# Kernel tuning notes

Hardware: AMD Instinct MI355X
Metric: run time of the kernel (lower is better)

The kernel has to match this reference:

```python
import jax, jax.numpy as jnp
import numpy as np

NUM_CLASSES = 80
TOPK = 9
EPS_OVERLAPS = 1e-6  # mmdet BboxOverlaps2D: union clamped to eps
EPS_YOLOV6 = 1e-9    # yolov6_iou_calculator: eps added to union


def _pairwise_iou(b1, b2, eps, add_eps):
    # b1: (..., M, 4), b2: (..., N, 4) xyxy -> (..., M, N)
    lt = jnp.maximum(b1[..., :, None, :2], b2[..., None, :, :2])
    rb = jnp.minimum(b1[..., :, None, 2:], b2[..., None, :, 2:])
    wh = jnp.clip(rb - lt, 0.0)
    overlap = wh[..., 0] * wh[..., 1]
    a1 = (b1[..., 2] - b1[..., 0]) * (b1[..., 3] - b1[..., 1])
    a2 = (b2[..., 2] - b2[..., 0]) * (b2[..., 3] - b2[..., 1])
    union = a1[..., :, None] + a2[..., None, :] - overlap
    return overlap / (union + eps) if add_eps else overlap / jnp.maximum(union, eps)


def _assign(pred_bboxes, priors, gt_labels, gt_bboxes, pad_bbox_flag, num_level_priors):
    num_level_priors = tuple(int(n) for n in np.asarray(num_level_priors))
    # priors (x, y, stride_w, stride_h) -> 5*stride cell boxes in xyxy
    cell_half = priors[:, 2:] * 2.5
    prior_boxes = jnp.concatenate([priors[:, :2] - cell_half, priors[:, :2] + cell_half], axis=-1)
    bs, num_gt = gt_bboxes.shape[0], gt_bboxes.shape[1]
    num_priors = priors.shape[0]
    gt_flat = gt_bboxes.reshape(-1, 4)

    # step 1: IoU between all priors and all gts
    overlaps = _pairwise_iou(gt_flat, prior_boxes, EPS_OVERLAPS, False).reshape(bs, num_gt, num_priors)

    # step 2: center distances
    gt_cxy = (gt_flat[:, :2] + gt_flat[:, 2:]) * 0.5
    prior_cxy = (prior_boxes[:, :2] + prior_boxes[:, 2:]) * 0.5
    dist = jnp.sqrt(jnp.sum((gt_cxy[:, None, :] - prior_cxy[None, :, :]) ** 2, axis=-1))
    dist = dist.reshape(bs, num_gt, num_priors)

    # step 3: per-level topk closest candidates
    pad_bool = pad_bbox_flag[..., 0] > 0  # (bs, num_gt)
    b_ix = jnp.arange(bs)[:, None, None]
    g_ix = jnp.arange(num_gt)[None, :, None]
    is_in_list, cand_list = [], []
    start = 0
    for pl in num_level_priors:
        k = min(TOPK, pl)
        d_l = jax.lax.dynamic_slice_in_dim(dist, start, pl, axis=-1)
        _, idx = jax.lax.top_k(-d_l, k)  # (bs, num_gt, k) smallest distances
        cand_list.append(idx + start)
        idx_m = jnp.where(pad_bool[..., None], idx, 0)
        counts = jnp.zeros((bs, num_gt, pl), dist.dtype).at[b_ix, g_ix, idx_m].add(1.0)
        is_in_list.append(jnp.where(counts > 1, jnp.zeros_like(counts), counts))
        start += pl
    is_in_candidate = jnp.concatenate(is_in_list, axis=-1)   # (bs, num_gt, num_priors)
    candidate_idxs = jnp.concatenate(cand_list, axis=-1)     # (bs, num_gt, k*levels)

    # step 4: mean + std of candidate IoUs as threshold
    candidate_overlaps = jnp.where(is_in_candidate > 0, overlaps, jnp.zeros_like(overlaps))
    gathered = jnp.take_along_axis(candidate_overlaps, candidate_idxs, axis=-1)
    thr = jnp.mean(gathered, axis=-1, keepdims=True) + jnp.std(gathered, axis=-1, keepdims=True, ddof=1)

    # step 5: keep candidates above threshold
    is_pos = jnp.where(candidate_overlaps > thr, is_in_candidate, jnp.zeros_like(is_in_candidate))

    # step 6: center of prior must lie inside gt box
    lt = prior_cxy[None, None, :, :] - gt_bboxes[:, :, None, :2]
    rb = gt_bboxes[:, :, None, 2:] - prior_cxy[None, None, :, :]
    is_in_gts = (jnp.minimum(lt, rb).min(axis=-1) > 1e-9).astype(gt_bboxes.dtype)

    pos_mask = is_pos * is_in_gts * pad_bbox_flag  # pad flag broadcasts (bs,num_gt,1)

    # resolve priors assigned to multiple gts: keep highest IoU gt
    fg = pos_mask.sum(axis=-2)  # (bs, num_priors)
    best_gt = jnp.argmax(overlaps, axis=1)  # (bs, num_priors)
    is_max = jax.nn.one_hot(best_gt, num_gt, dtype=pos_mask.dtype).transpose(0, 2, 1)
    pos_mask = jnp.where(fg[:, None, :] > 1, is_max, pos_mask)
    fg_mask = pos_mask.sum(axis=-2)                 # (bs, num_priors)
    gt_idx = jnp.argmax(pos_mask, axis=-2)          # (bs, num_priors)

    # targets
    flat_idx = gt_idx + jnp.arange(bs)[:, None] * num_gt
    assigned_labels = gt_labels.reshape(-1)[flat_idx]
    assigned_labels = jnp.where(fg_mask > 0, assigned_labels, NUM_CLASSES)
    assigned_bboxes = gt_bboxes.reshape(-1, 4)[flat_idx]
    assigned_scores = jax.nn.one_hot(assigned_labels, NUM_CLASSES + 1, dtype=gt_bboxes.dtype)[..., :NUM_CLASSES]

    # weight scores by IoU with predictions
    ious = _pairwise_iou(gt_bboxes, pred_bboxes, EPS_YOLOV6, True) * pos_mask
    assigned_scores = assigned_scores * jnp.max(ious, axis=-2)[..., None]
    return assigned_labels, assigned_bboxes, assigned_scores, fg_mask > 0


def setup_inputs() -> dict:
    key = jax.random.key(0)
    k0, k1, k2, k3, k4 = jax.random.split(key, 5)
    bs, num_gt, img = 32, 64, 640
    strides = (8, 16, 32)
    pri = []
    for s in strides:
        n = img // s
        xs = (np.arange(n, dtype=np.float32) + 0.5) * s
        gy, gx = np.meshgrid(xs, xs, indexing='ij')
        pts = np.stack([gx.ravel(), gy.ravel()], axis=1)
        st = np.full((pts.shape[0], 2), s, dtype=np.float32)
        pri.append(np.concatenate([pts, st], axis=1))
    priors = jnp.asarray(np.concatenate(pri, axis=0))  # (8400, 4)
    num_level_priors = (6400, 1600, 400)
    num_priors = priors.shape[0]
    cxy = jax.random.uniform(k0, (bs, num_gt, 2), minval=50.0, maxval=590.0)
    wh = jax.random.uniform(k1, (bs, num_gt, 2), minval=20.0, maxval=200.0)
    gt_bboxes = jnp.concatenate([cxy - wh * 0.5, cxy + wh * 0.5], axis=-1)
    gt_labels = jax.random.randint(k2, (bs, num_gt, 1), 0, NUM_CLASSES)
    pad_bbox_flag = jnp.ones((bs, num_gt, 1), jnp.float32)
    pcxy = priors[None, :, :2] + jax.random.normal(k3, (bs, num_priors, 2)) * 4.0
    pwh = jax.random.uniform(k4, (bs, num_priors, 2), minval=10.0, maxval=150.0)
    pred_bboxes = jnp.concatenate([pcxy - pwh * 0.5, pcxy + pwh * 0.5], axis=-1)
    return {'pred_bboxes': pred_bboxes, 'priors': priors, 'gt_labels': gt_labels,
            'gt_bboxes': gt_bboxes, 'pad_bbox_flag': pad_bbox_flag,
            'num_level_priors': num_level_priors}


def reference(pred_bboxes, priors, gt_labels, gt_bboxes, pad_bbox_flag, num_level_priors):
    return _assign(pred_bboxes, priors, gt_labels, gt_bboxes, pad_bbox_flag, num_level_priors)
```

## Files before the change

kernel.cpp:

```cpp
#include <hip/hip_runtime.h>

#define BS 32
#define NG 64
#define NP 8400
#define NTOPK 9
#define NUM_CLASSES 80
#define NCAND 27

__device__ __forceinline__ unsigned long long wave_min_u64(unsigned long long k) {
    #pragma unroll
    for (int off = 1; off < 64; off <<= 1) {
        unsigned long long o = __shfl_xor(k, off, 64);
        k = (o < k) ? o : k;
    }
    return k;
}

__global__ __launch_bounds__(256) void k_candidates(
    const float4* __restrict__ gt_bboxes,
    const float*  __restrict__ pad_flag,
    unsigned long long* __restrict__ posbits
) {
    const int bg   = (blockIdx.x * 256 + threadIdx.x) >> 6;
    const int lane = threadIdx.x & 63;
    const int b  = bg >> 6;
    const int g  = bg & 63;

    const float4 gt  = gt_bboxes[bg];
    const float  pad = pad_flag[bg];
    const float  gcx = (gt.x + gt.z) * 0.5f;
    const float  gcy = (gt.y + gt.w) * 0.5f;
    const float  garea = (gt.z - gt.x) * (gt.w - gt.y);

    const float lvl_s[3] = {8.0f, 16.0f, 32.0f};
    const int   lvl_n[3] = {80, 40, 20};
    const int   lvl_b[3] = {0, 6400, 8000};

    float ov[NCAND];
    int   ixs[NCAND];

    float sum = 0.0f;

    const int dy5 = lane / 5;
    const int dx5 = lane - dy5 * 5;

    #pragma unroll
    for (int L = 0; L < 3; ++L) {
        const float s    = lvl_s[L];
        const int   n    = lvl_n[L];
        const int   base = lvl_b[L];

        int wx = (int)floorf(gcx / s) - 2;
        int wy = (int)floorf(gcy / s) - 2;
        wx = min(max(wx, 0), n - 5);
        wy = min(max(wy, 0), n - 5);

        unsigned long long key = ~0ull;
        if (lane < 25) {
            const int   iy  = wy + dy5;
            const int   ix  = wx + dx5;
            const float py  = ((float)iy + 0.5f) * s;
            const float px  = ((float)ix + 0.5f) * s;
            const float ddx = gcx - px;
            const float ddy = gcy - py;
            const float d   = sqrtf(ddx * ddx + ddy * ddy);
            key = ((unsigned long long)__float_as_uint(d) << 32) |
                  (unsigned int)(base + iy * n + ix);
        }

        const float hx = s * 2.5f;
        #pragma unroll
        for (int q = 0; q < NTOPK; ++q) {
            const unsigned long long m = wave_min_u64(key);
            if (key == m) key = ~0ull;

            const int slot = L * NTOPK + q;
            const int idx  = (int)(m & 0xffffffffu);
            const int rel  = idx - base;
            const int iy   = rel / n;
            const int ix   = rel - iy * n;
            const float px = ((float)ix + 0.5f) * s;
            const float py = ((float)iy + 0.5f) * s;
            const float px0 = px - hx, py0 = py - hx;
            const float px1 = px + hx, py1 = py + hx;
            float lx = fmaxf(gt.x, px0), ly = fmaxf(gt.y, py0);
            float rx = fminf(gt.z, px1), ry = fminf(gt.w, py1);
            float w = fmaxf(rx - lx, 0.0f), h = fmaxf(ry - ly, 0.0f);
            float ovl = w * h;
            float parea = (px1 - px0) * (py1 - py0);
            float o = ovl / fmaxf(garea + parea - ovl, 1e-6f);
            ov[slot]  = o;
            ixs[slot] = idx;
            sum += o;
        }
    }

    const float mean = sum / (float)NCAND;
    float var = 0.0f;
    #pragma unroll
    for (int i = 0; i < NCAND; ++i) {
        float d = ov[i] - mean;
        var += d * d;
    }
    const float thr = mean + sqrtf(var / (float)(NCAND - 1));

    if (pad > 0.0f && lane == 0) {
        #pragma unroll
        for (int i = 0; i < NCAND; ++i) {
            if (ov[i] > thr) {
                const int   L    = i / NTOPK;
                const float s    = lvl_s[L];
                const int   n    = lvl_n[L];
                const int   base = lvl_b[L];
                const int idx = ixs[i];
                const int rel = idx - base;
                const int iy  = rel / n;
                const int ix  = rel - iy * n;
                const float px = ((float)ix + 0.5f) * s;
                const float py = ((float)iy + 0.5f) * s;
                float mm = fminf(fminf(px - gt.x, py - gt.y),
                                 fminf(gt.z - px, gt.w - py));
                if (mm > 1e-9f) {
                    atomicOr(&posbits[(size_t)b * NP + idx], 1ull << g);
                }
            }
        }
    }
}

__global__ __launch_bounds__(256) void k_assign(
    const float4* __restrict__ priors,
    const float4* __restrict__ gt_bboxes,
    const int*    __restrict__ gt_labels,
    const float4* __restrict__ pred_bboxes,
    const unsigned long long* __restrict__ posbits,
    float* __restrict__ out)
{
    __shared__ float4 s_gt[NG];
    __shared__ int    s_lab[NG];
    __shared__ int    s_plab[256];
    __shared__ float  s_piou[256];

    const int b   = blockIdx.y;
    const int tid = threadIdx.x;
    if (tid < NG) {
        s_gt[tid]  = gt_bboxes[b * NG + tid];
        s_lab[tid] = gt_labels[b * NG + tid];
    }
    __syncthreads();

    const int p0 = blockIdx.x * 256;
    const int p  = p0 + tid;
    int   label  = NUM_CLASSES;
    float iou_w  = 0.0f;

    if (p < NP) {
        const size_t bp = (size_t)b * NP + p;
        unsigned long long mask = posbits[bp];
        int fg = __popcll(mask);
        int gidx = 0;

        if (fg > 1) {
            float4 pr = priors[p];
            float hx = pr.z * 2.5f, hy = pr.w * 2.5f;
            float px0 = pr.x - hx, py0 = pr.y - hy, px1 = pr.x + hx, py1 = pr.y + hy;
            float parea = (px1 - px0) * (py1 - py0);
            float best = -1.0f;
            for (int gg = 0; gg < NG; ++gg) {
                float4 gtb = s_gt[gg];
                float lx = fmaxf(gtb.x, px0), ly = fmaxf(gtb.y, py0);
                float rx = fminf(gtb.z, px1), ry = fminf(gtb.w, py1);
                float w = fmaxf(rx - lx, 0.0f), h = fmaxf(ry - ly, 0.0f);
                float ovl = w * h;
                float ga = (gtb.z - gtb.x) * (gtb.w - gtb.y);
                float v = ovl / fmaxf(ga + parea - ovl, 1e-6f);
                if (v > best) { best = v; gidx = gg; }
            }
        } else if (fg == 1) {
            gidx = __ffsll((unsigned long long)mask) - 1;
        }

        const bool  fgm = fg > 0;
        const float4 gtb = s_gt[gidx];
        label = fgm ? s_lab[gidx] : NUM_CLASSES;

        if (fgm) {
            float4 pb = pred_bboxes[bp];
            float lx = fmaxf(gtb.x, pb.x), ly = fmaxf(gtb.y, pb.y);
            float rx = fminf(gtb.z, pb.z), ry = fminf(gtb.w, pb.w);
            float w = fmaxf(rx - lx, 0.0f), h = fmaxf(ry - ly, 0.0f);
            float ov = w * h;
            float ga = (gtb.z - gtb.x) * (gtb.w - gtb.y);
            float pa = (pb.z - pb.x) * (pb.w - pb.y);
            iou_w = ov / (ga + pa - ov + 1e-9f);
        }

        out[bp] = (float)label;
        ((float4*)(out + (size_t)BS * NP))[bp] = gtb;
        out[(size_t)BS * NP * 85 + bp] = fgm ? 1.0f : 0.0f;
    }

    s_plab[tid] = label;
    s_piou[tid] = iou_w;
    __syncthreads();

    const int npr  = min(256, NP - p0);
    const int nfl4 = npr * 20;
    float4* o4 = (float4*)(out + (size_t)BS * NP * 5 + ((size_t)b * NP + p0) * 80);
    for (int q = tid; q < nfl4; q += 256) {
        int pl   = q / 20;
        int comp = q - pl * 20;
        int lab  = s_plab[pl];
        float iw = s_piou[pl];
        int dd = lab - comp * 4;
        float4 v;
        v.x = (dd == 0) ? iw : 0.0f;
        v.y = (dd == 1) ? iw : 0.0f;
        v.z = (dd == 2) ? iw : 0.0f;
        v.w = (dd == 3) ? iw : 0.0f;
        o4[q] = v;
    }
}

extern "C" void kernel_launch(void* const* d_in, const int* in_sizes, int n_in,
                              void* d_out, int out_size, void* d_ws, size_t ws_size,
                              hipStream_t stream) {
    const float4* pred_bboxes = (const float4*)d_in[0];
    const float4* priors      = (const float4*)d_in[1];
    const int*    gt_labels   = (const int*)d_in[2];
    const float4* gt_bboxes   = (const float4*)d_in[3];
    const float*  pad_flag    = (const float*)d_in[4];

    unsigned long long* posbits = (unsigned long long*)d_ws;
    hipMemsetAsync(posbits, 0, (size_t)BS * NP * sizeof(unsigned long long), stream);

    k_candidates<<<dim3(BS * NG * 64 / 256), dim3(256), 0, stream>>>(
        gt_bboxes, pad_flag, posbits);

    k_assign<<<dim3((NP + 255) / 256, BS), dim3(256), 0, stream>>>(
        priors, gt_bboxes, gt_labels, pred_bboxes, posbits, (float*)d_out);
}
```

Before: 129.4 us.

## Fuse memset, candidate selection and assignment into one cooperative kernel

Replaces the memset plus two kernel launches with a single cooperative kernel. It zeroes the bitmask in-kernel, runs candidate selection, and after a grid-wide sync performs assignment on 525-prior chunks per block. The wave-min reduction is also narrowed to 32 lanes, since only 25 lanes hold keys. This removes launch and memset overhead at the cost of two grid syncs and a fixed 512-block grid, which must all be co-resident.

```diff
diff --git a/kernel.cpp b/kernel.cpp
--- a/kernel.cpp
+++ b/kernel.cpp
@@ -1,4 +1,7 @@
 #include <hip/hip_runtime.h>
+#include <hip/hip_cooperative_groups.h>
+
+namespace cg = cooperative_groups;
 
 #define BS 32
 #define NG 64
@@ -7,154 +10,161 @@
 #define NUM_CLASSES 80
 #define NCAND 27
 
-__device__ __forceinline__ unsigned long long wave_min_u64(unsigned long long k) {
+#define NBLK 512
+#define NTHR 256
+#define CHUNK 525
+
+__device__ __forceinline__ unsigned long long wave_min_u64_32(unsigned long long k) {
     #pragma unroll
-    for (int off = 1; off < 64; off <<= 1) {
+    for (int off = 1; off < 32; off <<= 1) {
         unsigned long long o = __shfl_xor(k, off, 64);
         k = (o < k) ? o : k;
     }
     return k;
 }
 
-__global__ __launch_bounds__(256) void k_candidates(
+__global__ __launch_bounds__(NTHR, 2) void k_fused(
     const float4* __restrict__ gt_bboxes,
     const float*  __restrict__ pad_flag,
-    unsigned long long* __restrict__ posbits
-) {
-    const int bg   = (blockIdx.x * 256 + threadIdx.x) >> 6;
-    const int lane = threadIdx.x & 63;
-    const int b  = bg >> 6;
-    const int g  = bg & 63;
-
-    const float4 gt  = gt_bboxes[bg];
-    const float  pad = pad_flag[bg];
-    const float  gcx = (gt.x + gt.z) * 0.5f;
-    const float  gcy = (gt.y + gt.w) * 0.5f;
-    const float  garea = (gt.z - gt.x) * (gt.w - gt.y);
-
-    const float lvl_s[3] = {8.0f, 16.0f, 32.0f};
-    const int   lvl_n[3] = {80, 40, 20};
-    const int   lvl_b[3] = {0, 6400, 8000};
-
-    float ov[NCAND];
-    int   ixs[NCAND];
-
-    float sum = 0.0f;
-
-    const int dy5 = lane / 5;
-    const int dx5 = lane - dy5 * 5;
-
-    #pragma unroll
-    for (int L = 0; L < 3; ++L) {
-        const float s    = lvl_s[L];
-        const int   n    = lvl_n[L];
-        const int   base = lvl_b[L];
-
-        int wx = (int)floorf(gcx / s) - 2;
-        int wy = (int)floorf(gcy / s) - 2;
-        wx = min(max(wx, 0), n - 5);
-        wy = min(max(wy, 0), n - 5);
-
-        unsigned long long key = ~0ull;
-        if (lane < 25) {
-            const int   iy  = wy + dy5;
-            const int   ix  = wx + dx5;
-            const float py  = ((float)iy + 0.5f) * s;
-            const float px  = ((float)ix + 0.5f) * s;
-            const float ddx = gcx - px;
-            const float ddy = gcy - py;
-            const float d   = sqrtf(ddx * ddx + ddy * ddy);
-            key = ((unsigned long long)__float_as_uint(d) << 32) |
-                  (unsigned int)(base + iy * n + ix);
-        }
-
-        const float hx = s * 2.5f;
+    const float4* __restrict__ priors,
+    const int*    __restrict__ gt_labels,
+    const float4* __restrict__ pred_bboxes,
+    unsigned long long* __restrict__ posbits,
+    float* __restrict__ out)
+{
+    cg::grid_group grid = cg::this_grid();
+
+    __shared__ float4 s_gt[NG];
+    __shared__ int    s_lab[NG];
+    __shared__ int    s_plab[CHUNK];
+    __shared__ float  s_piou[CHUNK];
+
+    const int tid  = threadIdx.x;
+    const int gtid = blockIdx.x * NTHR + tid;
+
+    for (int i = gtid; i < BS * NP; i += NBLK * NTHR) posbits[i] = 0;
+    grid.sync();
+
+    {
+        const int bg   = gtid >> 6;
+        const int lane = tid & 63;
+        const int b  = bg >> 6;
+        const int g  = bg & 63;
+
+        const float4 gt  = gt_bboxes[bg];
+        const float  pad = pad_flag[bg];
+        const float  gcx = (gt.x + gt.z) * 0.5f;
+        const float  gcy = (gt.y + gt.w) * 0.5f;
+        const float  garea = (gt.z - gt.x) * (gt.w - gt.y);
+
+        const float lvl_s[3] = {8.0f, 16.0f, 32.0f};
+        const int   lvl_n[3] = {80, 40, 20};
+        const int   lvl_b[3] = {0, 6400, 8000};
+
+        float ov[NCAND];
+        int   ixs[NCAND];
+        float sum = 0.0f;
+
+        const int dy5 = lane / 5;
+        const int dx5 = lane - dy5 * 5;
+
         #pragma unroll
-        for (int q = 0; q < NTOPK; ++q) {
-            const unsigned long long m = wave_min_u64(key);
-            if (key == m) key = ~0ull;
-
-            const int slot = L * NTOPK + q;
-            const int idx  = (int)(m & 0xffffffffu);
-            const int rel  = idx - base;
-            const int iy   = rel / n;
-            const int ix   = rel - iy * n;
-            const float px = ((float)ix + 0.5f) * s;
-            const float py = ((float)iy + 0.5f) * s;
-            const float px0 = px - hx, py0 = py - hx;
-            const float px1 = px + hx, py1 = py + hx;
-            float lx = fmaxf(gt.x, px0), ly = fmaxf(gt.y, py0);
-            float rx = fminf(gt.z, px1), ry = fminf(gt.w, py1);
-            float w = fmaxf(rx - lx, 0.0f), h = fmaxf(ry - ly, 0.0f);
-            float ovl = w * h;
-            float parea = (px1 - px0) * (py1 - py0);
-            float o = ovl / fmaxf(garea + parea - ovl, 1e-6f);
-            ov[slot]  = o;
-            ixs[slot] = idx;
-            sum += o;
-        }
-    }
-
-    const float mean = sum / (float)NCAND;
-    float var = 0.0f;
-    #pragma unroll
-    for (int i = 0; i < NCAND; ++i) {
-        float d = ov[i] - mean;
-        var += d * d;
-    }
-    const float thr = mean + sqrtf(var / (float)(NCAND - 1));
-
-    if (pad > 0.0f && lane == 0) {
+        for (int L = 0; L < 3; ++L) {
+            const float s    = lvl_s[L];
+            const int   n    = lvl_n[L];
+            const int   base = lvl_b[L];
+
+            int wx = (int)floorf(gcx / s) - 2;
+            int wy = (int)floorf(gcy / s) - 2;
+            wx = min(max(wx, 0), n - 5);
+            wy = min(max(wy, 0), n - 5);
+
+            unsigned long long key = ~0ull;
+            if (lane < 25) {
+                const int   iy  = wy + dy5;
+                const int   ix  = wx + dx5;
+                const float py  = ((float)iy + 0.5f) * s;
+                const float px  = ((float)ix + 0.5f) * s;
+                const float ddx = gcx - px;
+                const float ddy = gcy - py;
+                const float d   = sqrtf(ddx * ddx + ddy * ddy);
+                key = ((unsigned long long)__float_as_uint(d) << 32) |
+                      (unsigned int)(base + iy * n + ix);
+            }
+
+            const float hx = s * 2.5f;
+            #pragma unroll
+            for (int q = 0; q < NTOPK; ++q) {
+                const unsigned long long m = wave_min_u64_32(key);
+                if (key == m) key = ~0ull;
+
+                const int slot = L * NTOPK + q;
+                const int idx  = (int)(m & 0xffffffffu);
+                const int rel  = idx - base;
+                const int iy   = rel / n;
+                const int ix   = rel - iy * n;
+                const float px = ((float)ix + 0.5f) * s;
+                const float py = ((float)iy + 0.5f) * s;
+                const float px0 = px - hx, py0 = py - hx;
+                const float px1 = px + hx, py1 = py + hx;
+                float lx = fmaxf(gt.x, px0), ly = fmaxf(gt.y, py0);
+                float rx = fminf(gt.z, px1), ry = fminf(gt.w, py1);
+                float w = fmaxf(rx - lx, 0.0f), h = fmaxf(ry - ly, 0.0f);
+                float ovl = w * h;
+                float parea = (px1 - px0) * (py1 - py0);
+                float o = ovl / fmaxf(garea + parea - ovl, 1e-6f);
+                ov[slot]  = o;
+                ixs[slot] = idx;
+                sum += o;
+            }
+        }
+
+        const float mean = sum / (float)NCAND;
+        float var = 0.0f;
         #pragma unroll
         for (int i = 0; i < NCAND; ++i) {
-            if (ov[i] > thr) {
-                const int   L    = i / NTOPK;
-                const float s    = lvl_s[L];
-                const int   n    = lvl_n[L];
-                const int   base = lvl_b[L];
-                const int idx = ixs[i];
-                const int rel = idx - base;
-                const int iy  = rel / n;
-                const int ix  = rel - iy * n;
-                const float px = ((float)ix + 0.5f) * s;
-                const float py = ((float)iy + 0.5f) * s;
-                float mm = fminf(fminf(px - gt.x, py - gt.y),
-                                 fminf(gt.z - px, gt.w - py));
-                if (mm > 1e-9f) {
-                    atomicOr(&posbits[(size_t)b * NP + idx], 1ull << g);
+            float d = ov[i] - mean;
+            var += d * d;
+        }
+        const float thr = mean + sqrtf(var / (float)(NCAND - 1));
+
+        if (pad > 0.0f && lane == 0) {
+            #pragma unroll
+            for (int i = 0; i < NCAND; ++i) {
+                if (ov[i] > thr) {
+                    const int   L    = i / NTOPK;
+                    const float s    = lvl_s[L];
+                    const int   n    = lvl_n[L];
+                    const int   base = lvl_b[L];
+                    const int idx = ixs[i];
+                    const int rel = idx - base;
+                    const int iy  = rel / n;
+                    const int ix  = rel - iy * n;
+                    const float px = ((float)ix + 0.5f) * s;
+                    const float py = ((float)iy + 0.5f) * s;
+                    float mm = fminf(fminf(px - gt.x, py - gt.y),
+                                     fminf(gt.z - px, gt.w - py));
+                    if (mm > 1e-9f) {
+                        atomicOr(&posbits[(size_t)b * NP + idx], 1ull << g);
+                    }
                 }
             }
         }
     }
-}
-
-__global__ __launch_bounds__(256) void k_assign(
-    const float4* __restrict__ priors,
-    const float4* __restrict__ gt_bboxes,
-    const int*    __restrict__ gt_labels,
-    const float4* __restrict__ pred_bboxes,
-    const unsigned long long* __restrict__ posbits,
-    float* __restrict__ out)
-{
-    __shared__ float4 s_gt[NG];
-    __shared__ int    s_lab[NG];
-    __shared__ int    s_plab[256];
-    __shared__ float  s_piou[256];
-
-    const int b   = blockIdx.y;
-    const int tid = threadIdx.x;
+    grid.sync();
+
+    const int b     = blockIdx.x >> 4;
+    const int chunk = blockIdx.x & 15;
+    const int pbase = chunk * CHUNK;
+
     if (tid < NG) {
         s_gt[tid]  = gt_bboxes[b * NG + tid];
         s_lab[tid] = gt_labels[b * NG + tid];
     }
     __syncthreads();
 
-    const int p0 = blockIdx.x * 256;
-    const int p  = p0 + tid;
-    int   label  = NUM_CLASSES;
-    float iou_w  = 0.0f;
-
-    if (p < NP) {
+    for (int pl = tid; pl < CHUNK; pl += NTHR) {
+        const int p = pbase + pl;
         const size_t bp = (size_t)b * NP + p;
         unsigned long long mask = posbits[bp];
         int fg = __popcll(mask);
@@ -180,9 +190,10 @@
             gidx = __ffsll((unsigned long long)mask) - 1;
         }
 
-        const bool  fgm = fg > 0;
+        const bool   fgm = fg > 0;
         const float4 gtb = s_gt[gidx];
-        label = fgm ? s_lab[gidx] : NUM_CLASSES;
+        const int  label = fgm ? s_lab[gidx] : NUM_CLASSES;
+        float iou_w = 0.0f;
 
         if (fgm) {
             float4 pb = pred_bboxes[bp];
@@ -198,16 +209,14 @@
         out[bp] = (float)label;
         ((float4*)(out + (size_t)BS * NP))[bp] = gtb;
         out[(size_t)BS * NP * 85 + bp] = fgm ? 1.0f : 0.0f;
-    }
-
-    s_plab[tid] = label;
-    s_piou[tid] = iou_w;
+
+        s_plab[pl] = label;
+        s_piou[pl] = iou_w;
+    }
     __syncthreads();
 
-    const int npr  = min(256, NP - p0);
-    const int nfl4 = npr * 20;
-    float4* o4 = (float4*)(out + (size_t)BS * NP * 5 + ((size_t)b * NP + p0) * 80);
-    for (int q = tid; q < nfl4; q += 256) {
+    float4* o4 = (float4*)(out + (size_t)BS * NP * 5 + ((size_t)b * NP + pbase) * 80);
+    for (int q = tid; q < CHUNK * 20; q += NTHR) {
         int pl   = q / 20;
         int comp = q - pl * 20;
         int lab  = s_plab[pl];
@@ -232,11 +241,12 @@
     const float*  pad_flag    = (const float*)d_in[4];
 
     unsigned long long* posbits = (unsigned long long*)d_ws;
-    hipMemsetAsync(posbits, 0, (size_t)BS * NP * sizeof(unsigned long long), stream);
-
-    k_candidates<<<dim3(BS * NG * 64 / 256), dim3(256), 0, stream>>>(
-        gt_bboxes, pad_flag, posbits);
-
-    k_assign<<<dim3((NP + 255) / 256, BS), dim3(256), 0, stream>>>(
-        priors, gt_bboxes, gt_labels, pred_bboxes, posbits, (float*)d_out);
+    float* out = (float*)d_out;
+
+    void* args[] = {
+        (void*)&gt_bboxes, (void*)&pad_flag, (void*)&priors,
+        (void*)&gt_labels, (void*)&pred_bboxes, (void*)&posbits, (void*)&out
+    };
+    hipLaunchCooperativeKernel((const void*)k_fused, dim3(NBLK), dim3(NTHR),
+                               args, 0, stream);
 }
```

Result: slower. 230.9 us (+78.5%).

## Replace global posbits bitmask with compact candidate list scattered in shared memory

Applied to the files above, without the earlier changes.

The candidate kernel now writes a compact list of positive prior indices per gt (27 entries) instead of doing global atomicOr into a per-prior 64-bit mask. This removes the memset of the mask buffer and the global atomics. The assign kernel rebuilds each tile's masks in shared memory by scanning the whole candidate list for its batch, which adds redundant reads per block. The wave reduction also shrinks to 32 lanes, since only 25 lanes hold keys.

```diff
diff --git a/kernel.cpp b/kernel.cpp
--- a/kernel.cpp
+++ b/kernel.cpp
@@ -7,9 +7,9 @@
 #define NUM_CLASSES 80
 #define NCAND 27
 
-__device__ __forceinline__ unsigned long long wave_min_u64(unsigned long long k) {
+__device__ __forceinline__ unsigned long long wave_min_u64_32(unsigned long long k) {
     #pragma unroll
-    for (int off = 1; off < 64; off <<= 1) {
+    for (int off = 1; off < 32; off <<= 1) {
         unsigned long long o = __shfl_xor(k, off, 64);
         k = (o < k) ? o : k;
     }
@@ -19,12 +19,10 @@
 __global__ __launch_bounds__(256) void k_candidates(
     const float4* __restrict__ gt_bboxes,
     const float*  __restrict__ pad_flag,
-    unsigned long long* __restrict__ posbits
-) {
+    unsigned int* __restrict__ cand)
+{
     const int bg   = (blockIdx.x * 256 + threadIdx.x) >> 6;
     const int lane = threadIdx.x & 63;
-    const int b  = bg >> 6;
-    const int g  = bg & 63;
 
     const float4 gt  = gt_bboxes[bg];
     const float  pad = pad_flag[bg];
@@ -38,7 +36,6 @@
 
     float ov[NCAND];
     int   ixs[NCAND];
-
     float sum = 0.0f;
 
     const int dy5 = lane / 5;
@@ -71,7 +68,7 @@
         const float hx = s * 2.5f;
         #pragma unroll
         for (int q = 0; q < NTOPK; ++q) {
-            const unsigned long long m = wave_min_u64(key);
+            const unsigned long long m = wave_min_u64_32(key);
             if (key == m) key = ~0ull;
 
             const int slot = L * NTOPK + q;
@@ -104,9 +101,11 @@
     }
     const float thr = mean + sqrtf(var / (float)(NCAND - 1));
 
-    if (pad > 0.0f && lane == 0) {
+    unsigned int myval = 0xFFFFFFFFu;
+    if (pad > 0.0f) {
         #pragma unroll
         for (int i = 0; i < NCAND; ++i) {
+            bool pass = false;
             if (ov[i] > thr) {
                 const int   L    = i / NTOPK;
                 const float s    = lvl_s[L];
@@ -120,43 +119,56 @@
                 const float py = ((float)iy + 0.5f) * s;
                 float mm = fminf(fminf(px - gt.x, py - gt.y),
                                  fminf(gt.z - px, gt.w - py));
-                if (mm > 1e-9f) {
-                    atomicOr(&posbits[(size_t)b * NP + idx], 1ull << g);
-                }
+                pass = (mm > 1e-9f);
             }
-        }
-    }
-}
-
-__global__ __launch_bounds__(256) void k_assign(
+            if (lane == i && pass) myval = (unsigned int)ixs[i];
+        }
+    }
+    if (lane < NCAND) cand[(size_t)bg * NCAND + lane] = myval;
+}
+
+__global__ __launch_bounds__(256) void k_write(
     const float4* __restrict__ priors,
     const float4* __restrict__ gt_bboxes,
     const int*    __restrict__ gt_labels,
     const float4* __restrict__ pred_bboxes,
-    const unsigned long long* __restrict__ posbits,
+    const unsigned int* __restrict__ cand,
     float* __restrict__ out)
 {
     __shared__ float4 s_gt[NG];
     __shared__ int    s_lab[NG];
+    __shared__ unsigned long long s_pos[256];
     __shared__ int    s_plab[256];
     __shared__ float  s_piou[256];
 
     const int b   = blockIdx.y;
     const int tid = threadIdx.x;
+    const int p0  = blockIdx.x * 256;
+
     if (tid < NG) {
         s_gt[tid]  = gt_bboxes[b * NG + tid];
         s_lab[tid] = gt_labels[b * NG + tid];
     }
+    s_pos[tid] = 0;
     __syncthreads();
 
-    const int p0 = blockIdx.x * 256;
-    const int p  = p0 + tid;
+    const unsigned int* bc = cand + (size_t)b * NG * NCAND;
+    for (int e = tid; e < NG * NCAND; e += 256) {
+        unsigned int idx = bc[e];
+        unsigned int rel = idx - (unsigned int)p0;
+        if (rel < 256u) {
+            atomicOr(&s_pos[rel], 1ull << (e / NCAND));
+        }
+    }
+    __syncthreads();
+
+    const int p = p0 + tid;
     int   label  = NUM_CLASSES;
     float iou_w  = 0.0f;
 
     if (p < NP) {
         const size_t bp = (size_t)b * NP + p;
-        unsigned long long mask = posbits[bp];
+        unsigned long long mask = s_pos[tid];
         int fg = __popcll(mask);
         int gidx = 0;
 
@@ -180,7 +192,7 @@
             gidx = __ffsll((unsigned long long)mask) - 1;
         }
 
-        const bool  fgm = fg > 0;
+        const bool   fgm = fg > 0;
         const float4 gtb = s_gt[gidx];
         label = fgm ? s_lab[gidx] : NUM_CLASSES;
 
@@ -231,12 +243,11 @@
     const float4* gt_bboxes   = (const float4*)d_in[3];
     const float*  pad_flag    = (const float*)d_in[4];
 
-    unsigned long long* posbits = (unsigned long long*)d_ws;
-    hipMemsetAsync(posbits, 0, (size_t)BS * NP * sizeof(unsigned long long), stream);
+    unsigned int* cand = (unsigned int*)d_ws;
 
     k_candidates<<<dim3(BS * NG * 64 / 256), dim3(256), 0, stream>>>(
-        gt_bboxes, pad_flag, posbits);
-
-    k_assign<<<dim3((NP + 255) / 256, BS), dim3(256), 0, stream>>>(
-        priors, gt_bboxes, gt_labels, pred_bboxes, posbits, (float*)d_out);
-}
+        gt_bboxes, pad_flag, cand);
+
+    k_write<<<dim3((NP + 255) / 256, BS), dim3(256), 0, stream>>>(
+        priors, gt_bboxes, gt_labels, pred_bboxes, cand, (float*)d_out);
+}
```

New measurement: 125.1 us. -3.3%, faster.
